# Performance work log

Hardware: AMD Instinct MI355X
Metric: run time of the kernel (lower is better)

## Reference

```python
import jax, jax.numpy as jnp
import numpy as np
from jax import lax

B, L, D, H, OM = 16, 512, 2048, 512, 5


def _lstm(seq, wih, whh, bih, bhh):
    # seq: [T, B, F]; PyTorch gate order i, f, g, o
    Hh = whh.shape[1]
    Bb = seq.shape[1]
    def step(carry, xt):
        h, c = carry
        g = xt @ wih.T + h @ whh.T + bih + bhh
        i, f, gg, o = jnp.split(g, 4, axis=-1)
        c = jax.nn.sigmoid(f) * c + jax.nn.sigmoid(i) * jnp.tanh(gg)
        h = jax.nn.sigmoid(o) * jnp.tanh(c)
        return (h, c), h
    z = jnp.zeros((Bb, Hh), seq.dtype)
    _, hs = lax.scan(step, (z, z), seq)
    return hs  # [T, B, Hh]


def setup_inputs() -> dict:
    key = jax.random.key(0)
    ks = jax.random.split(key, 17)
    s = 0.02
    f32 = jnp.float32
    inp = {
        "x": jax.random.normal(ks[0], (B, L, D), f32),
        "wb": jax.random.normal(ks[1], (H, D, OM), f32) * s,
        "bb": jax.random.normal(ks[2], (H,), f32) * s,
        "wa": jax.random.normal(ks[3], (H, D, OM), f32) * s,
        "ba": jax.random.normal(ks[4], (H,), f32) * s,
        "wr": jax.random.normal(ks[5], (H, D, 2 * OM), f32) * s,
        "br": jax.random.normal(ks[6], (H,), f32) * s,
        "wih_f": jax.random.normal(ks[7], (4 * H, H + 1), f32) * s,
        "whh_f": jax.random.normal(ks[8], (4 * H, H), f32) * s,
        "bih_f": jax.random.normal(ks[9], (4 * H,), f32) * s,
        "bhh_f": jax.random.normal(ks[10], (4 * H,), f32) * s,
        "wih_r": jax.random.normal(ks[11], (4 * H, H + 1), f32) * s,
        "whh_r": jax.random.normal(ks[12], (4 * H, H), f32) * s,
        "bih_r": jax.random.normal(ks[13], (4 * H,), f32) * s,
        "bhh_r": jax.random.normal(ks[14], (4 * H,), f32) * s,
        "wfc": jax.random.normal(ks[15], (1, 2 * H), f32) * s,
        "bfc": jax.random.normal(ks[16], (1,), f32) * s,
    }
    return inp


def reference(x, wb, bb, wa, ba, wr, br, wih_f, whh_f, bih_f, bhh_f,
              wih_r, whh_r, bih_r, bhh_r, wfc, bfc):
    om = OM
    xc = jnp.transpose(x, (0, 2, 1))  # [B, D, L]
    conv = lambda w, b: lax.conv_general_dilated(
        xc, w, (1,), 'VALID', dimension_numbers=('NCH', 'OIH', 'NCH')) + b[None, :, None]
    cb = conv(wb, bb)  # [B, H, L-om+1]
    ca = conv(wa, ba)  # [B, H, L-om+1]
    cr = conv(wr, br)  # [B, H, L-2om+1]
    T = x.shape[1] - 2 * om  # number of centers c in [om, L-om)
    d_before = cb[:, :, 0:T]          # window [c-om, c) == conv output c-om
    d_after = ca[:, :, om:om + T]     # window [c, c+om) == conv output c
    vts_d = jnp.sum(d_before * d_after, axis=1, keepdims=True)  # [B, 1, T]
    vts_r = cr[:, :, 0:T]             # full window; pool over length-1 is identity
    vts_seq = jnp.concatenate([vts_r, vts_d], axis=1)  # [B, H+1, T]
    seq = jnp.transpose(vts_seq, (2, 0, 1))  # [T, B, H+1]
    hs_f = _lstm(seq, wih_f, whh_f, bih_f, bhh_f)
    hs_r = _lstm(seq[::-1], wih_r, whh_r, bih_r, bhh_r)[::-1]
    h = jnp.concatenate([hs_f, hs_r], axis=-1)  # [T, B, 2H]
    logits = jnp.einsum('tbh,h->tb', h, wfc[0]) + bfc[0]
    return jax.nn.sigmoid(jnp.transpose(logits))  # [B, T]
```

## Files before the change

kernel.cpp:

```cpp
#include <hip/hip_runtime.h>
#include <hip/hip_bf16.h>

typedef short v8s __attribute__((ext_vector_type(8)));
typedef float v4f __attribute__((ext_vector_type(4)));
typedef unsigned int u32;
typedef unsigned short u16;
typedef unsigned long long u64;

__device__ __forceinline__ u16 f2bf(float f) {
    union { float f; u32 u; } x; x.f = f;
    u32 r = x.u + 0x7fffu + ((x.u >> 16) & 1u);
    return (u16)(r >> 16);
}
__device__ __forceinline__ float bf2f(u16 s) {
    union { u32 u; float f; } x; x.u = ((u32)s) << 16;
    return x.f;
}
__device__ __forceinline__ float sigmoidf_(float x) { return 1.f / (1.f + __expf(-x)); }
__device__ __forceinline__ float tanh_fast(float x) {
    float t = fminf(fmaxf(x, -15.f), 15.f);
    float e = __expf(2.f * t);
    return (e - 1.f) / (e + 1.f);
}

__global__ __launch_bounds__(256) void xbf_kernel(const float* __restrict__ x, u16* __restrict__ xbf, int n) {
    int i = (blockIdx.x * 256 + threadIdx.x) * 4;
    if (i + 3 < n) {
        float4 v = *(const float4*)(x + i);
        u16* d = xbf + i;
        d[0] = f2bf(v.x); d[1] = f2bf(v.y); d[2] = f2bf(v.z); d[3] = f2bf(v.w);
    }
}

__global__ __launch_bounds__(256) void packw_kernel(const float* __restrict__ wb, const float* __restrict__ wa,
                                                    const float* __restrict__ wr, u16* __restrict__ W1, u16* __restrict__ W2) {
    long idx = (long)blockIdx.x * 256 + threadIdx.x;
    int which = idx >= (1024L * 10240) ? 1 : 0;
    long rem = idx - (long)which * 1024 * 10240;
    int n = (int)(rem / 10240);
    int kap = (int)(rem % 10240);
    int tap = kap >> 11, d = kap & 2047;
    float v;
    if (n < 512) v = which ? wa[(long)n * 10240 + d * 5 + tap] : wb[(long)n * 10240 + d * 5 + tap];
    else         v = wr[(long)(n - 512) * 20480 + d * 10 + tap + (which ? 5 : 0)];
    (which ? W2 : W1)[rem] = f2bf(v);
}

__global__ __launch_bounds__(256) void packwih_kernel(const float* __restrict__ wf, const float* __restrict__ wr,
                                                      u16* __restrict__ Bp) {
    int idx = blockIdx.x * 256 + threadIdx.x;
    int n = idx / 576, kap = idx % 576;
    int dir = n >> 11, g = n & 2047;
    const float* src = dir ? wr : wf;
    float v = (kap < 513) ? src[(long)g * 513 + kap] : 0.f;
    Bp[idx] = f2bf(v);
}

__global__ __launch_bounds__(256) void packwhh_kernel(const float* __restrict__ whf, const float* __restrict__ whr,
                                                      u16* __restrict__ W) {
    int idx = blockIdx.x * 256 + threadIdx.x;
    int dir = idx >> 20;
    float v = dir ? whr[idx & 1048575] : whf[idx];
    W[idx] = f2bf(v);
}

__global__ __launch_bounds__(256) void misc_kernel(const float* __restrict__ bihf, const float* __restrict__ bhhf,
                                                   const float* __restrict__ bihr, const float* __restrict__ bhhr,
                                                   float* __restrict__ bsum, u64* __restrict__ hbuf) {
    int i = blockIdx.x * 256 + threadIdx.x;
    if (i < 2048) bsum[i] = bihf[i] + bhhf[i];
    else if (i < 4096) bsum[i] = bihr[i - 2048] + bhhr[i - 2048];
    else if (i < 4096 + 16384) hbuf[i - 4096] = 0xFFFFFFFF00000000ULL;
}

template <int OUTBF>
__global__ __launch_bounds__(256) void gemm_bf16(const u16* __restrict__ A, const u16* __restrict__ B,
                                                 void* __restrict__ Cv, int M, int N, int K, int ldc,
                                                 int row_div, u32 row_mul1, u32 row_mul2, u32 row_base) {
    __shared__ u16 ldsA[128 * 64];
    __shared__ u16 ldsB[128 * 64];
    const int ntn = N >> 7;
    const int tm = blockIdx.x / ntn, tn = blockIdx.x % ntn;
    const int tid = threadIdx.x, lane = tid & 63, wv = tid >> 6;
    const int wm = wv >> 1, wn = wv & 1;
    const int qbase = wv * 4;

    u32 asrc[4], bsrc[4];
#pragma unroll
    for (int it = 0; it < 4; ++it) {
        int q = qbase + it;
        int r = q * 8 + (lane >> 3);
        int cb = ((lane & 7) * 16) ^ ((r & 7) << 4);
        int m = tm * 128 + r; if (m > M - 1) m = M - 1;
        asrc[it] = row_base + (u32)(m / row_div) * row_mul1 + (u32)(m % row_div) * row_mul2 + (u32)(cb >> 1);
        int n = tn * 128 + r;
        bsrc[it] = (u32)n * (u32)K + (u32)(cb >> 1);
    }

    v4f acc[4][4];
#pragma unroll
    for (int i = 0; i < 4; ++i)
#pragma unroll
        for (int j = 0; j < 4; ++j) acc[i][j] = (v4f){0.f, 0.f, 0.f, 0.f};

    const int KT = K >> 6;
    for (int kt = 0; kt < KT; ++kt) {
        const int k0 = kt << 6;
#pragma unroll
        for (int it = 0; it < 4; ++it) {
            int q = qbase + it;
            __builtin_amdgcn_global_load_lds(
                (const __attribute__((address_space(1))) u32*)(A + asrc[it] + k0),
                (__attribute__((address_space(3))) u32*)((char*)ldsA + q * 1024), 16, 0, 0);
            __builtin_amdgcn_global_load_lds(
                (const __attribute__((address_space(1))) u32*)(B + bsrc[it] + k0),
                (__attribute__((address_space(3))) u32*)((char*)ldsB + q * 1024), 16, 0, 0);
        }
        __syncthreads();
#pragma unroll
        for (int kk = 0; kk < 2; ++kk) {
            v8s af[4], bfr[4];
#pragma unroll
            for (int i = 0; i < 4; ++i) {
                int row = wm * 64 + i * 16 + (lane & 15);
                int cbyte = (kk * 64 + ((lane >> 4) * 16)) ^ ((row & 7) << 4);
                af[i] = *(const v8s*)((const char*)ldsA + row * 128 + cbyte);
                int rn = wn * 64 + i * 16 + (lane & 15);
                int cbn = (kk * 64 + ((lane >> 4) * 16)) ^ ((rn & 7) << 4);
                bfr[i] = *(const v8s*)((const char*)ldsB + rn * 128 + cbn);
            }
#pragma unroll
            for (int i = 0; i < 4; ++i)
#pragma unroll
                for (int j = 0; j < 4; ++j)
                    acc[i][j] = __builtin_amdgcn_mfma_f32_16x16x32_bf16(af[i], bfr[j], acc[i][j], 0, 0, 0);
        }
        __syncthreads();
    }
#pragma unroll
    for (int i = 0; i < 4; ++i)
#pragma unroll
        for (int j = 0; j < 4; ++j)
#pragma unroll
            for (int r = 0; r < 4; ++r) {
                int m = tm * 128 + wm * 64 + i * 16 + (lane >> 4) * 4 + r;
                int n = tn * 128 + wn * 64 + j * 16 + (lane & 15);
                if (m < M) {
                    if (OUTBF) ((u16*)Cv)[(long)m * ldc + n] = f2bf(acc[i][j][r]);
                    else       ((float*)Cv)[(long)m * ldc + n] = acc[i][j][r];
                }
            }
}

__global__ __launch_bounds__(256) void combine_kernel(const float* __restrict__ G1, const float* __restrict__ G2,
                                                      const float* __restrict__ bb, const float* __restrict__ ba,
                                                      const float* __restrict__ br, u16* __restrict__ seqpad) {
    int m = blockIdx.x;
    int b = m / 502, t = m % 502;
    int tid = threadIdx.x;
    const float* g1 = G1 + (long)m * 1024;
    const float* g2 = G2 + (long)m * 1024;
    u16* dst = seqpad + (long)(t * 16 + b) * 576;
    float part = 0.f;
#pragma unroll
    for (int rep = 0; rep < 2; ++rep) {
        int u = tid + rep * 256;
        float db = g1[u] + bb[u];
        float da = g2[u] + ba[u];
        part += db * da;
        float vr = g1[512 + u] + g2[512 + u] + br[u];
        dst[u] = f2bf(vr);
    }
#pragma unroll
    for (int off = 32; off; off >>= 1) part += __shfl_down(part, off, 64);
    __shared__ float red[4];
    if ((tid & 63) == 0) red[tid >> 6] = part;
    __syncthreads();
    if (tid == 0) dst[512] = f2bf(red[0] + red[1] + red[2] + red[3]);
    if (tid >= 1 && tid < 64) dst[512 + tid] = 0;
}

__global__ __launch_bounds__(256, 1) void lstm_kernel(const u16* __restrict__ P, const u16* __restrict__ whhbf,
                                                      const float* __restrict__ bsum, u64* hbuf,
                                                      u16* __restrict__ hs) {
    const int wg = blockIdx.x;
    const int dir = wg >> 4, j = wg & 15;
    const int tid = threadIdx.x, lane = tid & 63, w = tid >> 6;
    __shared__ u16 hls[16 * 512];
    __shared__ float gls[4][16][32];

    v8s bf[2][16];
    const u16* whd = whhbf + (long)dir * 2048 * 512;
#pragma unroll
    for (int nt = 0; nt < 2; ++nt) {
        int n = w * 512 + j * 32 + nt * 16 + (lane & 15);
#pragma unroll
        for (int kt = 0; kt < 16; ++kt)
            bf[nt][kt] = *(const v8s*)(whd + (long)n * 512 + kt * 32 + ((lane >> 4) * 8));
    }

    for (int i = tid; i < 8192; i += 256) hls[i] = 0;

    const int b_ = tid >> 4;
    const int u_ = (tid * 2) & 31;
    float c0 = 0.f, c1 = 0.f;
    u64* hb = hbuf + dir * 2 * 4096;

    const int col0 = w * 512 + j * 32 + (lane & 15);
    const float bs0 = bsum[dir * 2048 + col0];
    const float bs1 = bsum[dir * 2048 + col0 + 16];
    const u16* Pd = P + dir * 2048;

    float pv[2][4];
    {
        int tau = dir ? 501 : 0;
#pragma unroll
        for (int nt = 0; nt < 2; ++nt)
#pragma unroll
            for (int r = 0; r < 4; ++r) {
                int b = (lane >> 4) * 4 + r;
                pv[nt][r] = bf2f(Pd[(long)(tau * 16 + b) * 4096 + col0 + nt * 16]);
            }
    }
    __syncthreads();

    for (int s = 0; s < 502; ++s) {
        const int tau = dir ? (501 - s) : s;
        if (s > 0) {
            const u64* slot = hb + ((s - 1) & 1) * 4096;
            const u32 want = (u32)(s - 1);
            u64 vv[16];
            for (;;) {
                u32 ok = 0;
#pragma unroll
                for (int rep = 0; rep < 16; ++rep)
                    vv[rep] = __hip_atomic_load(slot + tid + rep * 256, __ATOMIC_RELAXED, __HIP_MEMORY_SCOPE_AGENT);
#pragma unroll
                for (int rep = 0; rep < 16; ++rep)
                    ok += ((u32)(vv[rep] >> 32) == want);
                if (ok == 16) break;
            }
#pragma unroll
            for (int rep = 0; rep < 16; ++rep) {
                int i = tid + rep * 256;
                int b = i >> 8;
                int byteoff = (b << 10) + (((i & 255) << 2) ^ ((b & 7) << 4));
                *(u32*)((char*)hls + byteoff) = (u32)vv[rep];
            }
            __syncthreads();
        }
        v4f acc[2];
#pragma unroll
        for (int nt = 0; nt < 2; ++nt)
#pragma unroll
            for (int r = 0; r < 4; ++r)
                acc[nt][r] = pv[nt][r] + (nt ? bs1 : bs0);
#pragma unroll
        for (int kt = 0; kt < 16; ++kt) {
            int row = lane & 15;
            int cbyte = (kt * 64 + ((lane >> 4) * 16)) ^ ((row & 7) << 4);
            v8s af = *(const v8s*)((const char*)hls + row * 1024 + cbyte);
            acc[0] = __builtin_amdgcn_mfma_f32_16x16x32_bf16(af, bf[0][kt], acc[0], 0, 0, 0);
            acc[1] = __builtin_amdgcn_mfma_f32_16x16x32_bf16(af, bf[1][kt], acc[1], 0, 0, 0);
        }
#pragma unroll
        for (int nt = 0; nt < 2; ++nt)
#pragma unroll
            for (int r = 0; r < 4; ++r)
                gls[w][(lane >> 4) * 4 + r][nt * 16 + (lane & 15)] = acc[nt][r];
        __syncthreads();

        float i0 = gls[0][b_][u_],     f0 = gls[1][b_][u_],     g0 = gls[2][b_][u_],     o0 = gls[3][b_][u_];
        float i1 = gls[0][b_][u_ + 1], f1 = gls[1][b_][u_ + 1], g1v = gls[2][b_][u_ + 1], o1 = gls[3][b_][u_ + 1];
        c0 = sigmoidf_(f0) * c0 + sigmoidf_(i0) * tanh_fast(g0);
        c1 = sigmoidf_(f1) * c1 + sigmoidf_(i1) * tanh_fast(g1v);
        float h0 = sigmoidf_(o0) * tanh_fast(c0);
        float h1 = sigmoidf_(o1) * tanh_fast(c1);
        u32 hw = (u32)f2bf(h0) | ((u32)f2bf(h1) << 16);
        int gi = (b_ * 512 + j * 32 + u_) >> 1;
        __hip_atomic_store(hb + (s & 1) * 4096 + gi, (u64)hw | ((u64)(u32)s << 32),
                           __ATOMIC_RELAXED, __HIP_MEMORY_SCOPE_AGENT);
        *(u32*)(hs + (((long)(dir * 502 + tau) * 16 + b_) * 512 + j * 32 + u_)) = hw;
        if (s + 1 < 502) {
            int tau2 = dir ? (500 - s) : (s + 1);
#pragma unroll
            for (int nt = 0; nt < 2; ++nt)
#pragma unroll
                for (int r = 0; r < 4; ++r) {
                    int b = (lane >> 4) * 4 + r;
                    pv[nt][r] = bf2f(Pd[(long)(tau2 * 16 + b) * 4096 + col0 + nt * 16]);
                }
        }
        __syncthreads();
    }
}

__global__ __launch_bounds__(256) void final_kernel(const u16* __restrict__ hs, const float* __restrict__ wfc,
                                                    const float* __restrict__ bfc, float* __restrict__ out) {
    int m = blockIdx.x;
    int t = m >> 4, b = m & 15;
    int tid = threadIdx.x;
    const u16* hf = hs + ((long)t * 16 + b) * 512;
    const u16* hr = hs + ((long)(502 + t) * 16 + b) * 512;
    float part = 0.f;
#pragma unroll
    for (int rep = 0; rep < 2; ++rep) {
        int u = tid + rep * 256;
        part += bf2f(hf[u]) * wfc[u] + bf2f(hr[u]) * wfc[512 + u];
    }
#pragma unroll
    for (int off = 32; off; off >>= 1) part += __shfl_down(part, off, 64);
    __shared__ float red[4];
    if ((tid & 63) == 0) red[tid >> 6] = part;
    __syncthreads();
    if (tid == 0) {
        float lg = red[0] + red[1] + red[2] + red[3] + bfc[0];
        out[(long)b * 502 + t] = 1.f / (1.f + __expf(-lg));
    }
}

extern "C" void kernel_launch(void* const* d_in, const int* in_sizes, int n_in,
                              void* d_out, int out_size, void* d_ws, size_t ws_size,
                              hipStream_t stream) {
    const float* x     = (const float*)d_in[0];
    const float* wb    = (const float*)d_in[1];
    const float* bb    = (const float*)d_in[2];
    const float* wa    = (const float*)d_in[3];
    const float* ba    = (const float*)d_in[4];
    const float* wr    = (const float*)d_in[5];
    const float* br    = (const float*)d_in[6];
    const float* wih_f = (const float*)d_in[7];
    const float* whh_f = (const float*)d_in[8];
    const float* bih_f = (const float*)d_in[9];
    const float* bhh_f = (const float*)d_in[10];
    const float* wih_r = (const float*)d_in[11];
    const float* whh_r = (const float*)d_in[12];
    const float* bih_r = (const float*)d_in[13];
    const float* bhh_r = (const float*)d_in[14];
    const float* wfc   = (const float*)d_in[15];
    const float* bfc   = (const float*)d_in[16];
    float* out = (float*)d_out;

    char* ws = (char*)d_ws;
    u16* xbf = (u16*)ws;
    u16* W1  = (u16*)(ws + 33554432);
    u16* W2  = (u16*)(ws + 54525952);
    u16* Pb  = (u16*)ws;
    char* r2 = ws + 75497472;
    float* G1 = (float*)r2;
    float* G2 = (float*)(r2 + 32899072);
    u16*  hs  = (u16*)r2;
    char* r3 = r2 + 65798144;
    u16*  seqp = (u16*)r3;
    u16*  wihp = (u16*)(r3 + 9252864);
    u16*  whhb = (u16*)(r3 + 13971456);
    float* bsum= (float*)(r3 + 18165760);
    u64*  hbuf = (u64*)(r3 + 18182144);

    xbf_kernel<<<16384, 256, 0, stream>>>(x, xbf, 16 * 512 * 2048);
    packw_kernel<<<81920, 256, 0, stream>>>(wb, wa, wr, W1, W2);
    packwih_kernel<<<9216, 256, 0, stream>>>(wih_f, wih_r, wihp);
    packwhh_kernel<<<8192, 256, 0, stream>>>(whh_f, whh_r, whhb);
    misc_kernel<<<80, 256, 0, stream>>>(bih_f, bhh_f, bih_r, bhh_r, bsum, hbuf);

    gemm_bf16<0><<<63 * 8, 256, 0, stream>>>(xbf, W1, G1, 8032, 1024, 10240, 1024,
                                             502, 512u * 2048u, 2048u, 0u);
    gemm_bf16<0><<<63 * 8, 256, 0, stream>>>(xbf, W2, G2, 8032, 1024, 10240, 1024,
                                             502, 512u * 2048u, 2048u, 5u * 2048u);
    combine_kernel<<<8032, 256, 0, stream>>>(G1, G2, bb, ba, br, seqp);
    gemm_bf16<1><<<63 * 32, 256, 0, stream>>>(seqp, wihp, Pb, 8032, 4096, 576, 4096,
                                              8032, 0u, 576u, 0u);
    lstm_kernel<<<32, 256, 0, stream>>>(Pb, whhb, bsum, hbuf, hs);
    final_kernel<<<8032, 256, 0, stream>>>(hs, wfc, bfc, out);
}
```

Before: 1.787 ms.

## Restructure LSTM across fewer workgroups, vectorize weight packing, swizzle GEMM tiles

The LSTM recurrence now runs on 16 workgroups instead of 32. Each wave owns all four gates for its hidden units, so the gate nonlinearity runs directly in registers and the LDS gate exchange and its extra barrier are gone. The cross-workgroup h polling uses wide inline-asm dwordx4 loads with sc1 in place of many 64-bit atomic loads, which cuts per-step sync latency but makes each workgroup do twice the MFMA work and hold twice the Whh registers. Separately, the weight-pack kernel converts four elements per thread, and the bf16 GEMM remaps block IDs to improve L2 locality.

```diff
diff --git a/kernel.cpp b/kernel.cpp
--- a/kernel.cpp
+++ b/kernel.cpp
@@ -4,6 +4,7 @@
 typedef short v8s __attribute__((ext_vector_type(8)));
 typedef float v4f __attribute__((ext_vector_type(4)));
 typedef unsigned int u32;
+typedef unsigned int u32x4 __attribute__((ext_vector_type(4)));
 typedef unsigned short u16;
 typedef unsigned long long u64;
 
@@ -34,16 +35,23 @@
 
 __global__ __launch_bounds__(256) void packw_kernel(const float* __restrict__ wb, const float* __restrict__ wa,
                                                     const float* __restrict__ wr, u16* __restrict__ W1, u16* __restrict__ W2) {
-    long idx = (long)blockIdx.x * 256 + threadIdx.x;
-    int which = idx >= (1024L * 10240) ? 1 : 0;
-    long rem = idx - (long)which * 1024 * 10240;
+    long e = ((long)blockIdx.x * 256 + threadIdx.x) * 4;
+    int which = e >= (1024L * 10240) ? 1 : 0;
+    long rem = e - (long)which * 1024 * 10240;
     int n = (int)(rem / 10240);
     int kap = (int)(rem % 10240);
     int tap = kap >> 11, d = kap & 2047;
-    float v;
-    if (n < 512) v = which ? wa[(long)n * 10240 + d * 5 + tap] : wb[(long)n * 10240 + d * 5 + tap];
-    else         v = wr[(long)(n - 512) * 20480 + d * 10 + tap + (which ? 5 : 0)];
-    (which ? W2 : W1)[rem] = f2bf(v);
+    u16 o[4];
+    if (n < 512) {
+        const float* src = which ? wa : wb;
+#pragma unroll
+        for (int q = 0; q < 4; ++q) o[q] = f2bf(src[(long)n * 10240 + (d + q) * 5 + tap]);
+    } else {
+        const float* src = wr + (long)(n - 512) * 20480 + tap + (which ? 5 : 0);
+#pragma unroll
+        for (int q = 0; q < 4; ++q) o[q] = f2bf(src[(d + q) * 10]);
+    }
+    *(u64*)((which ? W2 : W1) + rem) = *(const u64*)o;
 }
 
 __global__ __launch_bounds__(256) void packwih_kernel(const float* __restrict__ wf, const float* __restrict__ wr,
@@ -80,7 +88,10 @@
     __shared__ u16 ldsA[128 * 64];
     __shared__ u16 ldsB[128 * 64];
     const int ntn = N >> 7;
-    const int tm = blockIdx.x / ntn, tn = blockIdx.x % ntn;
+    const int nwg = gridDim.x;
+    const int bid = blockIdx.x;
+    const int swz = (bid & 7) * (nwg >> 3) + (bid >> 3);
+    const int tm = swz / ntn, tn = swz % ntn;
     const int tid = threadIdx.x, lane = tid & 63, wv = tid >> 6;
     const int wm = wv >> 1, wn = wv & 1;
     const int qbase = wv * 4;
@@ -184,112 +195,130 @@
                                                       const float* __restrict__ bsum, u64* hbuf,
                                                       u16* __restrict__ hs) {
     const int wg = blockIdx.x;
-    const int dir = wg >> 4, j = wg & 15;
+    const int dir = wg >> 3, j = wg & 7;
     const int tid = threadIdx.x, lane = tid & 63, w = tid >> 6;
     __shared__ u16 hls[16 * 512];
-    __shared__ float gls[4][16][32];
-
-    v8s bf[2][16];
+
+    v8s bf[4][16];
     const u16* whd = whhbf + (long)dir * 2048 * 512;
 #pragma unroll
-    for (int nt = 0; nt < 2; ++nt) {
-        int n = w * 512 + j * 32 + nt * 16 + (lane & 15);
+    for (int nt = 0; nt < 4; ++nt) {
+        int n = nt * 512 + j * 64 + w * 16 + (lane & 15);
 #pragma unroll
         for (int kt = 0; kt < 16; ++kt)
             bf[nt][kt] = *(const v8s*)(whd + (long)n * 512 + kt * 32 + ((lane >> 4) * 8));
     }
-
     for (int i = tid; i < 8192; i += 256) hls[i] = 0;
 
-    const int b_ = tid >> 4;
-    const int u_ = (tid * 2) & 31;
-    float c0 = 0.f, c1 = 0.f;
+    float c[4] = {0.f, 0.f, 0.f, 0.f};
     u64* hb = hbuf + dir * 2 * 4096;
-
-    const int col0 = w * 512 + j * 32 + (lane & 15);
-    const float bs0 = bsum[dir * 2048 + col0];
-    const float bs1 = bsum[dir * 2048 + col0 + 16];
+    const int colbase = j * 64 + w * 16 + (lane & 15);
+    float bs[4];
+#pragma unroll
+    for (int nt = 0; nt < 4; ++nt) bs[nt] = bsum[dir * 2048 + nt * 512 + colbase];
     const u16* Pd = P + dir * 2048;
 
-    float pv[2][4];
+    float pv[4][4];
     {
         int tau = dir ? 501 : 0;
 #pragma unroll
-        for (int nt = 0; nt < 2; ++nt)
-#pragma unroll
-            for (int r = 0; r < 4; ++r) {
-                int b = (lane >> 4) * 4 + r;
-                pv[nt][r] = bf2f(Pd[(long)(tau * 16 + b) * 4096 + col0 + nt * 16]);
-            }
+        for (int nt = 0; nt < 4; ++nt)
+#pragma unroll
+            for (int r = 0; r < 4; ++r)
+                pv[nt][r] = bf2f(Pd[(long)(tau * 16 + ((lane >> 4) * 4 + r)) * 4096 + nt * 512 + colbase]);
     }
     __syncthreads();
 
     for (int s = 0; s < 502; ++s) {
         const int tau = dir ? (501 - s) : s;
         if (s > 0) {
-            const u64* slot = hb + ((s - 1) & 1) * 4096;
+            const u64* slotp = hb + ((s - 1) & 1) * 4096;
             const u32 want = (u32)(s - 1);
-            u64 vv[16];
+            u64 base = (u64)slotp + (u64)tid * 16;
+            u64 a0 = base,          a1 = base + 4096,  a2 = base + 8192,  a3 = base + 12288;
+            u64 a4 = base + 16384,  a5 = base + 20480, a6 = base + 24576, a7 = base + 28672;
+            u32x4 w0, w1, w2, w3, w4, w5, w6, w7;
             for (;;) {
-                u32 ok = 0;
-#pragma unroll
-                for (int rep = 0; rep < 16; ++rep)
-                    vv[rep] = __hip_atomic_load(slot + tid + rep * 256, __ATOMIC_RELAXED, __HIP_MEMORY_SCOPE_AGENT);
-#pragma unroll
-                for (int rep = 0; rep < 16; ++rep)
-                    ok += ((u32)(vv[rep] >> 32) == want);
+                asm volatile(
+                    "global_load_dwordx4 %[w0], %[a0], off sc1\n\t"
+                    "global_load_dwordx4 %[w1], %[a1], off sc1\n\t"
+                    "global_load_dwordx4 %[w2], %[a2], off sc1\n\t"
+                    "global_load_dwordx4 %[w3], %[a3], off sc1\n\t"
+                    "global_load_dwordx4 %[w4], %[a4], off sc1\n\t"
+                    "global_load_dwordx4 %[w5], %[a5], off sc1\n\t"
+                    "global_load_dwordx4 %[w6], %[a6], off sc1\n\t"
+                    "global_load_dwordx4 %[w7], %[a7], off sc1\n\t"
+                    "s_waitcnt vmcnt(0)"
+                    : [w0]"=v"(w0), [w1]"=v"(w1), [w2]"=v"(w2), [w3]"=v"(w3),
+                      [w4]"=v"(w4), [w5]"=v"(w5), [w6]"=v"(w6), [w7]"=v"(w7)
+                    : [a0]"v"(a0), [a1]"v"(a1), [a2]"v"(a2), [a3]"v"(a3),
+                      [a4]"v"(a4), [a5]"v"(a5), [a6]"v"(a6), [a7]"v"(a7)
+                    : "memory");
+                u32 ok = (w0[1] == want) + (w0[3] == want) + (w1[1] == want) + (w1[3] == want)
+                       + (w2[1] == want) + (w2[3] == want) + (w3[1] == want) + (w3[3] == want)
+                       + (w4[1] == want) + (w4[3] == want) + (w5[1] == want) + (w5[3] == want)
+                       + (w6[1] == want) + (w6[3] == want) + (w7[1] == want) + (w7[3] == want);
                 if (ok == 16) break;
             }
-#pragma unroll
-            for (int rep = 0; rep < 16; ++rep) {
-                int i = tid + rep * 256;
-                int b = i >> 8;
-                int byteoff = (b << 10) + (((i & 255) << 2) ^ ((b & 7) << 4));
-                *(u32*)((char*)hls + byteoff) = (u32)vv[rep];
-            }
-            __syncthreads();
-        }
-        v4f acc[2];
-#pragma unroll
-        for (int nt = 0; nt < 2; ++nt)
-#pragma unroll
-            for (int r = 0; r < 4; ++r)
-                acc[nt][r] = pv[nt][r] + (nt ? bs1 : bs0);
+#define FILL(rep, pay0, pay1) {                                                             \
+            int i0 = tid * 2 + (rep) * 512;                                                 \
+            int bb2 = i0 >> 8; int p = i0 & 255;                                            \
+            int bo = (bb2 << 10) + ((p << 2) ^ ((bb2 & 7) << 4));                           \
+            *(u32*)((char*)hls + bo) = (pay0);                                              \
+            int i1 = i0 + 1; int p1 = i1 & 255;                                             \
+            int bo1 = (bb2 << 10) + ((p1 << 2) ^ ((bb2 & 7) << 4));                         \
+            *(u32*)((char*)hls + bo1) = (pay1); }
+            FILL(0, w0[0], w0[2]) FILL(1, w1[0], w1[2]) FILL(2, w2[0], w2[2]) FILL(3, w3[0], w3[2])
+            FILL(4, w4[0], w4[2]) FILL(5, w5[0], w5[2]) FILL(6, w6[0], w6[2]) FILL(7, w7[0], w7[2])
+#undef FILL
+        }
+        __syncthreads();
+        v4f a0, a1, a2, a3;
+#pragma unroll
+        for (int r = 0; r < 4; ++r) {
+            a0[r] = pv[0][r] + bs[0]; a1[r] = pv[1][r] + bs[1];
+            a2[r] = pv[2][r] + bs[2]; a3[r] = pv[3][r] + bs[3];
+        }
 #pragma unroll
         for (int kt = 0; kt < 16; ++kt) {
             int row = lane & 15;
-            int cbyte = (kt * 64 + ((lane >> 4) * 16)) ^ ((row & 7) << 4);
-            v8s af = *(const v8s*)((const char*)hls + row * 1024 + cbyte);
-            acc[0] = __builtin_amdgcn_mfma_f32_16x16x32_bf16(af, bf[0][kt], acc[0], 0, 0, 0);
-            acc[1] = __builtin_amdgcn_mfma_f32_16x16x32_bf16(af, bf[1][kt], acc[1], 0, 0, 0);
-        }
-#pragma unroll
-        for (int nt = 0; nt < 2; ++nt)
-#pragma unroll
-            for (int r = 0; r < 4; ++r)
-                gls[w][(lane >> 4) * 4 + r][nt * 16 + (lane & 15)] = acc[nt][r];
-        __syncthreads();
-
-        float i0 = gls[0][b_][u_],     f0 = gls[1][b_][u_],     g0 = gls[2][b_][u_],     o0 = gls[3][b_][u_];
-        float i1 = gls[0][b_][u_ + 1], f1 = gls[1][b_][u_ + 1], g1v = gls[2][b_][u_ + 1], o1 = gls[3][b_][u_ + 1];
-        c0 = sigmoidf_(f0) * c0 + sigmoidf_(i0) * tanh_fast(g0);
-        c1 = sigmoidf_(f1) * c1 + sigmoidf_(i1) * tanh_fast(g1v);
-        float h0 = sigmoidf_(o0) * tanh_fast(c0);
-        float h1 = sigmoidf_(o1) * tanh_fast(c1);
-        u32 hw = (u32)f2bf(h0) | ((u32)f2bf(h1) << 16);
-        int gi = (b_ * 512 + j * 32 + u_) >> 1;
-        __hip_atomic_store(hb + (s & 1) * 4096 + gi, (u64)hw | ((u64)(u32)s << 32),
-                           __ATOMIC_RELAXED, __HIP_MEMORY_SCOPE_AGENT);
-        *(u32*)(hs + (((long)(dir * 502 + tau) * 16 + b_) * 512 + j * 32 + u_)) = hw;
+            int cb = (kt * 64 + ((lane >> 4) * 16)) ^ ((row & 7) << 4);
+            v8s af = *(const v8s*)((const char*)hls + row * 1024 + cb);
+            a0 = __builtin_amdgcn_mfma_f32_16x16x32_bf16(af, bf[0][kt], a0, 0, 0, 0);
+            a1 = __builtin_amdgcn_mfma_f32_16x16x32_bf16(af, bf[1][kt], a1, 0, 0, 0);
+            a2 = __builtin_amdgcn_mfma_f32_16x16x32_bf16(af, bf[2][kt], a2, 0, 0, 0);
+            a3 = __builtin_amdgcn_mfma_f32_16x16x32_bf16(af, bf[3][kt], a3, 0, 0, 0);
+        }
+        u32 mine[4];
+#pragma unroll
+        for (int r = 0; r < 4; ++r) {
+            c[r] = sigmoidf_(a1[r]) * c[r] + sigmoidf_(a0[r]) * tanh_fast(a2[r]);
+            mine[r] = (u32)f2bf(sigmoidf_(a3[r]) * tanh_fast(c[r]));
+        }
+        u32 nb0 = (u32)__shfl_xor((int)mine[0], 1, 64);
+        u32 nb1 = (u32)__shfl_xor((int)mine[1], 1, 64);
+        u32 nb2 = (u32)__shfl_xor((int)mine[2], 1, 64);
+        u32 nb3 = (u32)__shfl_xor((int)mine[3], 1, 64);
+        if (!(lane & 1)) {
+            int wordbase = j * 32 + w * 8 + ((lane & 15) >> 1);
+            u64* slot = hb + (s & 1) * 4096;
+            u16* hrow = hs + ((long)(dir * 502 + tau) * 16) * 512 + j * 64 + w * 16 + (lane & 15);
+#pragma unroll
+            for (int r = 0; r < 4; ++r) {
+                int b = (lane >> 4) * 4 + r;
+                u32 hw = mine[r] | ((r == 0 ? nb0 : r == 1 ? nb1 : r == 2 ? nb2 : nb3) << 16);
+                __hip_atomic_store(slot + b * 256 + wordbase, (u64)hw | ((u64)(u32)s << 32),
+                                   __ATOMIC_RELAXED, __HIP_MEMORY_SCOPE_AGENT);
+                *(u32*)(hrow + (long)b * 512) = hw;
+            }
+        }
         if (s + 1 < 502) {
             int tau2 = dir ? (500 - s) : (s + 1);
 #pragma unroll
-            for (int nt = 0; nt < 2; ++nt)
-#pragma unroll
-                for (int r = 0; r < 4; ++r) {
-                    int b = (lane >> 4) * 4 + r;
-                    pv[nt][r] = bf2f(Pd[(long)(tau2 * 16 + b) * 4096 + col0 + nt * 16]);
-                }
+            for (int nt = 0; nt < 4; ++nt)
+#pragma unroll
+                for (int r = 0; r < 4; ++r)
+                    pv[nt][r] = bf2f(Pd[(long)(tau2 * 16 + ((lane >> 4) * 4 + r)) * 4096 + nt * 512 + colbase]);
         }
         __syncthreads();
     }
@@ -358,7 +387,7 @@
     u64*  hbuf = (u64*)(r3 + 18182144);
 
     xbf_kernel<<<16384, 256, 0, stream>>>(x, xbf, 16 * 512 * 2048);
-    packw_kernel<<<81920, 256, 0, stream>>>(wb, wa, wr, W1, W2);
+    packw_kernel<<<20480, 256, 0, stream>>>(wb, wa, wr, W1, W2);
     packwih_kernel<<<9216, 256, 0, stream>>>(wih_f, wih_r, wihp);
     packwhh_kernel<<<8192, 256, 0, stream>>>(whh_f, whh_r, whhb);
     misc_kernel<<<80, 256, 0, stream>>>(bih_f, bhh_f, bih_r, bhh_r, bsum, hbuf);
@@ -370,6 +399,6 @@
     combine_kernel<<<8032, 256, 0, stream>>>(G1, G2, bb, ba, br, seqp);
     gemm_bf16<1><<<63 * 32, 256, 0, stream>>>(seqp, wihp, Pb, 8032, 4096, 576, 4096,
                                               8032, 0u, 576u, 0u);
-    lstm_kernel<<<32, 256, 0, stream>>>(Pb, whhb, bsum, hbuf, hs);
+    lstm_kernel<<<16, 256, 0, stream>>>(Pb, whhb, bsum, hbuf, hs);
     final_kernel<<<8032, 256, 0, stream>>>(hs, wfc, bfc, out);
 }
```

Measured after the change: 2.285 ms. +27.9%, slower.
